# Optimization experiments

Measured on AMD Instinct MI355X. Metric: run time of the kernel, lower is better.

The kernel has to match this reference:

```python
import jax, jax.numpy as jnp
import numpy as np

# 5x5 binomial Gaussian kernel, normalized by 256
_K = jnp.array([[1., 4., 6., 4., 1.],
                [4., 16., 24., 16., 4.],
                [6., 24., 36., 24., 6.],
                [4., 16., 24., 16., 4.],
                [1., 4., 6., 4., 1.]], dtype=jnp.float32) / 256.0


def _gauss_conv(img, kernel):
    # depthwise 5x5 conv with reflect padding 2 (same spatial size)
    C = img.shape[1]
    p = jnp.pad(img, ((0, 0), (0, 0), (2, 2), (2, 2)), mode='reflect')
    return jax.lax.conv_general_dilated(
        p, kernel, window_strides=(1, 1), padding='VALID',
        dimension_numbers=('NCHW', 'OIHW', 'NCHW'),
        feature_group_count=C)


def _lap_pyramid(img, kernel, max_levels=5):
    pyr = []
    cur = img
    for _ in range(max_levels):  # fixed small loop over pyramid levels
        H, W = cur.shape[2], cur.shape[3]
        cur = cur[:, :, :H - H % 2, :W - W % 2]  # crop to even size
        down = _gauss_conv(cur, kernel)[:, :, ::2, ::2]
        up = jnp.zeros(cur.shape, cur.dtype).at[:, :, ::2, ::2].set(down * 4.0)
        up = _gauss_conv(up, kernel)
        pyr.append(cur - up)
        cur = down
    return pyr


def setup_inputs() -> dict:
    key = jax.random.key(0)
    k1, k2 = jax.random.split(key)
    predict = jax.random.uniform(k1, (16, 3, 512, 512), dtype=jnp.float32)
    target = jax.random.uniform(k2, (16, 3, 512, 512), dtype=jnp.float32)
    return {"predict": predict, "target": target}


def reference(predict, target):
    C = predict.shape[1]
    kernel = jnp.tile(_K.astype(predict.dtype)[None, None], (C, 1, 1, 1))  # [C,1,5,5]
    pyr_p = _lap_pyramid(predict, kernel, 5)
    pyr_t = _lap_pyramid(target, kernel, 5)
    weights = (1.0, 2.0, 4.0, 8.0, 16.0)
    loss = jnp.asarray(0.0, predict.dtype)
    for w, a, b in zip(weights, pyr_p, pyr_t):
        loss = loss + w * jnp.mean(jnp.abs(a - b))  # F.l1_loss (mean reduction)
    return loss
```

## Files before the change

### kernel.cpp

```cpp
#include <hip/hip_runtime.h>


__device__ __forceinline__ int reflect_i(int m, int S) {
    if (m < 0) m = -m;
    if (m >= S) m = 2 * S - 2 - m;
    return m;
}

__device__ __forceinline__ void wg_barrier() {
    asm volatile("s_waitcnt lgkmcnt(0)" ::: "memory");
    __builtin_amdgcn_s_barrier();
}

#define LGKM0 asm volatile("s_waitcnt lgkmcnt(0)" ::: "memory")

template <int N>
__device__ __forceinline__ void wait_vm() {
    if constexpr (N == 0)      asm volatile("s_waitcnt vmcnt(0)" ::: "memory");
    else if constexpr (N == 1) asm volatile("s_waitcnt vmcnt(1)" ::: "memory");
    else if constexpr (N == 2) asm volatile("s_waitcnt vmcnt(2)" ::: "memory");
    else if constexpr (N == 4) asm volatile("s_waitcnt vmcnt(4)" ::: "memory");
    else if constexpr (N == 8) asm volatile("s_waitcnt vmcnt(8)" ::: "memory");
}

__device__ __forceinline__ void gld16(const void* g, void* l) {
    __builtin_amdgcn_global_load_lds(
        (const __attribute__((address_space(1))) void*)g,
        (__attribute__((address_space(3))) void*)l, 16, 0, 0);
}

__device__ __forceinline__ int swz4(int B) { return B ^ (((B >> 7) & 7) << 4); }

template <int S, int ISL0, int DH>
__global__ __launch_bounds__(256, 2)
void pyr_kernel(const float* __restrict__ a, const float* __restrict__ b,
                float* __restrict__ dwn, float* __restrict__ acc, float scale) {
    constexpr int D = S / 2;
    constexpr int CPL = S / 128;
    constexpr int W = 2 * CPL + 3;
    constexpr int ROWB = (CPL == 4) ? 2048 : 1024;
    constexpr int SLOT = ROWB * (ISL0 ? 2 : 1);
    constexpr int OPS = (CPL == 4) ? (ISL0 ? 4 : 2) : 1;
    constexpr int NRS = D / DH;

    __shared__ float4 ringmem[4 * 4 * SLOT / 16];
    const int wv = threadIdx.x >> 6;
    const int lane = threadIdx.x & 63;
    char* ring = (char*)ringmem + wv * (4 * SLOT);

    const int wid = blockIdx.x * 4 + wv;
    const int rs = wid % NRS;
    const int n = wid / NRS;
    const int R0 = rs * DH;
    const size_t gbase = (size_t)n * S * S;

    auto stage_row = [&](int s) {
        int gr = reflect_i(2 * R0 - 4 + s, S);
        const char* ga = (const char*)(a + gbase + (size_t)gr * S);
        char* la = ring + (s & 3) * SLOT;
        if constexpr (CPL == 4) {
            gld16(ga + swz4(16 * lane), la);
            gld16(ga + swz4(16 * lane + 1024), la + 1024);
        } else if constexpr (CPL == 2) {
            gld16(ga + 16 * lane, la);
        } else {
            gld16(ga + 16 * (lane & 31), la);
        }
        if constexpr (ISL0) {
            const char* gb = (const char*)(b + gbase + (size_t)gr * S);
            gld16(gb + swz4(16 * lane), la + ROWB);
            gld16(gb + swz4(16 * lane + 1024), la + ROWB + 1024);
        }
    };

    auto read_win = [&](int s, float* w) {
        const char* pa = ring + (s & 3) * SLOT;
        if constexpr (CPL == 4) {
            int bl = 32 * lane;
            float2 lo = *(const float2*)(pa + swz4(lane ? bl - 8 : 0));
            float4 m0 = *(const float4*)(pa + swz4(bl));
            float4 m1 = *(const float4*)(pa + swz4(bl + 16));
            float hi = *(const float*)(pa + swz4(lane == 63 ? 2032 : bl + 32));
            w[0]=lo.x; w[1]=lo.y; w[2]=m0.x; w[3]=m0.y; w[4]=m0.z; w[5]=m0.w;
            w[6]=m1.x; w[7]=m1.y; w[8]=m1.z; w[9]=m1.w; w[10]=hi;
            if constexpr (ISL0) {
                const char* pb = pa + ROWB;
                float2 l2 = *(const float2*)(pb + swz4(lane ? bl - 8 : 0));
                float4 t0 = *(const float4*)(pb + swz4(bl));
                float4 t1 = *(const float4*)(pb + swz4(bl + 16));
                float h2 = *(const float*)(pb + swz4(lane == 63 ? 2032 : bl + 32));
                w[0]-=l2.x; w[1]-=l2.y; w[2]-=t0.x; w[3]-=t0.y; w[4]-=t0.z;
                w[5]-=t0.w; w[6]-=t1.x; w[7]-=t1.y; w[8]-=t1.z; w[9]-=t1.w; w[10]-=h2;
            }
        } else if constexpr (CPL == 2) {
            int bl = 16 * lane;
            float2 lo = *(const float2*)(pa + (lane ? bl - 8 : 0));
            float4 m0 = *(const float4*)(pa + bl);
            float hi = *(const float*)(pa + (lane == 63 ? 1008 : bl + 16));
            w[0]=lo.x; w[1]=lo.y; w[2]=m0.x; w[3]=m0.y; w[4]=m0.z; w[5]=m0.w; w[6]=hi;
        } else {
            int bl = 8 * lane;
            float2 lo = *(const float2*)(pa + (lane ? bl - 8 : 0));
            float2 m0 = *(const float2*)(pa + bl);
            float hi = *(const float*)(pa + (lane == 63 ? 496 : bl + 8));
            w[0]=lo.x; w[1]=lo.y; w[2]=m0.x; w[3]=m0.y; w[4]=hi;
        }
        if (lane == 0)  { w[0] = w[4]; w[1] = w[3]; }
        if (lane == 63) { w[W - 1] = w[W - 3]; }
    };

    auto hof = [&](const float* w, float* h) {
        #pragma unroll
        for (int j = 0; j < CPL; j++)
            h[j] = w[2*j] + 4.f*w[2*j+1] + 6.f*w[2*j+2] + 4.f*w[2*j+3] + w[2*j+4];
    };

    float hA[CPL], hB[CPL], hC[CPL], hD[CPL], hE[CPL];
    float cEv1[2*CPL], cEv2[2*CPL], cOd1[2*CPL];
    float ex0[CPL] = {}, ex1[CPL] = {}, ox0[CPL] = {}, ox1[CPL] = {};
    float sum = 0.f;
    float* dbase = dwn + (size_t)n * D * D;

    stage_row(0); stage_row(1); stage_row(2); stage_row(3);
    wait_vm<OPS>();
    {
        float w[W];
        read_win(0, w); hof(w, hA);
        read_win(1, w); hof(w, hB);
        read_win(2, w); hof(w, hC);
    }
    LGKM0;
    stage_row(4); stage_row(5); stage_row(6);

    #pragma unroll
    for (int j = 0; j <= DH + 1; ++j) {
        const int m = R0 - 1 + j;
        if (j <= DH) wait_vm<2 * OPS>(); else wait_vm<0>();

        float w3[W], w4[W];
        read_win(2 * j + 3, w3); hof(w3, hD);
        read_win(2 * j + 4, w4); hof(w4, hE);

        float d[CPL], dl[CPL], dr[CPL], ex2[CPL], ox2[CPL];
        #pragma unroll
        for (int q = 0; q < CPL; q++)
            d[q] = (hA[q] + 4.f*hB[q] + 6.f*hC[q] + 4.f*hD[q] + hE[q]) * (1.f / 256.f);
        float dli = __shfl_up(d[CPL - 1], 1, 64);
        float dri = __shfl_down(d[0], 1, 64);
        dl[0] = (lane == 0) ? ((CPL > 1) ? d[1] : dri) : dli;
        #pragma unroll
        for (int q = 1; q < CPL; q++) dl[q] = d[q - 1];
        dr[CPL - 1] = (lane == 63) ? d[CPL - 1] : dri;
        #pragma unroll
        for (int q = 0; q < CPL - 1; q++) dr[q] = d[q + 1];
        #pragma unroll
        for (int q = 0; q < CPL; q++) {
            ex2[q] = 0.125f * (dl[q] + 6.f * d[q] + dr[q]);
            ox2[q] = 0.5f * (d[q] + dr[q]);
        }

        if (j >= 1 && j <= DH) {
            char* dst = (char*)(dbase + (size_t)m * D + CPL * lane);
            if constexpr (CPL == 4)      *(float4*)dst = make_float4(d[0], d[1], d[2], d[3]);
            else if constexpr (CPL == 2) *(float2*)dst = make_float2(d[0], d[1]);
            else                         *(float*)dst = d[0];
        }

        if (j >= 2) {
            const int me = m - 1;
            #pragma unroll
            for (int q = 0; q < CPL; q++) {
                float eA = (me == 0) ? ex2[q] : ex0[q];
                float oA = (me == 0) ? ox2[q] : ox0[q];
                float eC = (me == D - 1) ? ex1[q] : ex2[q];
                float oC = (me == D - 1) ? ox1[q] : ox2[q];
                float uee = 0.125f * (eA + 6.f * ex1[q] + eC);
                float ueo = 0.125f * (oA + 6.f * ox1[q] + oC);
                float uoe = 0.5f * (ex1[q] + eC);
                float uoo = 0.5f * (ox1[q] + oC);
                sum += fabsf(cEv2[2*q]   - uee) + fabsf(cEv2[2*q+1] - ueo)
                     + fabsf(cOd1[2*q]   - uoe) + fabsf(cOd1[2*q+1] - uoo);
            }
        }

        #pragma unroll
        for (int q = 0; q < CPL; q++) {
            ex0[q] = ex1[q]; ex1[q] = ex2[q];
            ox0[q] = ox1[q]; ox1[q] = ox2[q];
            hA[q] = hC[q]; hB[q] = hD[q]; hC[q] = hE[q];
        }
        #pragma unroll
        for (int q = 0; q < 2 * CPL; q++) {
            cEv2[q] = cEv1[q];
            cEv1[q] = w4[2 + q];
            cOd1[q] = w3[2 + q];
        }

        if (j <= DH - 1) {
            LGKM0;
            stage_row(2 * j + 7);
            stage_row(2 * j + 8);
        }
    }

    #pragma unroll
    for (int o = 32; o > 0; o >>= 1) sum += __shfl_down(sum, o, 64);
    if (lane == 0) atomicAdd(&acc[wid & 63], sum * scale);
}

__device__ float level_in_lds(const float* cur, float* h, float* dn,
                              int S, int tid, int nt) {
    const int D = S >> 1;
    for (int i = tid; i < S * D; i += nt) {
        int r = i / D, xh = i % D;
        int c0 = reflect_i(2 * xh - 2, S), c1 = reflect_i(2 * xh - 1, S);
        int c3 = 2 * xh + 1, c4 = reflect_i(2 * xh + 2, S);
        const float* row = cur + r * S;
        h[i] = row[c0] + 4.f * row[c1] + 6.f * row[2 * xh] + 4.f * row[c3] + row[c4];
    }
    wg_barrier();
    for (int i = tid; i < D * D; i += nt) {
        int yh = i / D, xh = i % D;
        int r0 = reflect_i(2 * yh - 2, S), r1 = reflect_i(2 * yh - 1, S);
        int r3 = 2 * yh + 1, r4 = reflect_i(2 * yh + 2, S);
        dn[i] = (h[r0 * D + xh] + 4.f * h[r1 * D + xh] + 6.f * h[2 * yh * D + xh]
               + 4.f * h[r3 * D + xh] + h[r4 * D + xh]) * (1.f / 256.f);
    }
    wg_barrier();
    float sum = 0.f;
    for (int i = tid; i < D * D; i += nt) {
        int yh2 = i / D, q = i % D;
        int rm = (yh2 == 0) ? 1 : yh2 - 1;
        int rp = (yh2 == D - 1) ? D - 1 : yh2 + 1;
        int cm = (q == 0) ? 1 : q - 1;
        int cp = (q == D - 1) ? D - 1 : q + 1;
        float A00 = dn[rm * D + cm], A01 = dn[rm * D + q], A02 = dn[rm * D + cp];
        float A10 = dn[yh2 * D + cm], A11 = dn[yh2 * D + q], A12 = dn[yh2 * D + cp];
        float A20 = dn[rp * D + cm], A21 = dn[rp * D + q], A22 = dn[rp * D + cp];
        float ex0 = (A00 + 6.f * A01 + A02) * 0.125f;
        float ex1 = (A10 + 6.f * A11 + A12) * 0.125f;
        float ex2 = (A20 + 6.f * A21 + A22) * 0.125f;
        float ox0 = (A01 + A02) * 0.5f;
        float ox1 = (A11 + A12) * 0.5f;
        float ox2 = (A21 + A22) * 0.5f;
        float uee = (ex0 + 6.f * ex1 + ex2) * 0.125f;
        float ueo = (ox0 + 6.f * ox1 + ox2) * 0.125f;
        float uoe = (ex1 + ex2) * 0.5f;
        float uoo = (ox1 + ox2) * 0.5f;
        const float* c0 = cur + (2 * yh2) * S + 2 * q;
        sum += fabsf(c0[0] - uee) + fabsf(c0[1] - ueo)
             + fabsf(c0[S] - uoe) + fabsf(c0[S + 1] - uoo);
    }
    wg_barrier();
    return sum;
}

__global__ __launch_bounds__(256)
void tail_kernel(const float* __restrict__ d2, float* __restrict__ acc,
                 float s3, float s4) {
    __shared__ float cur[64 * 64];
    __shared__ float hbuf[64 * 32];
    __shared__ float dn3[32 * 32];
    __shared__ float dn4[16 * 16];
    int n = blockIdx.x, tid = threadIdx.x;
    const float4* src = (const float4*)(d2 + (size_t)n * 64 * 64);
    for (int i = tid; i < 64 * 16; i += 256) ((float4*)cur)[i] = src[i];
    wg_barrier();
    float sum = level_in_lds(cur, hbuf, dn3, 64, tid, 256) * s3;
    sum += level_in_lds(dn3, hbuf, dn4, 32, tid, 256) * s4;
    #pragma unroll
    for (int o = 32; o > 0; o >>= 1) sum += __shfl_down(sum, o, 64);
    __shared__ float s[4];
    int lane = tid & 63, w = tid >> 6;
    if (lane == 0) s[w] = sum;
    wg_barrier();
    if (tid == 0) atomicAdd(&acc[n & 63], s[0] + s[1] + s[2] + s[3]);
}

__global__ void finish_kernel(const float* __restrict__ acc, float* __restrict__ out) {
    float v = acc[threadIdx.x];
    #pragma unroll
    for (int o = 32; o > 0; o >>= 1) v += __shfl_down(v, o, 64);
    if (threadIdx.x == 0) out[0] = v;
}

extern "C" void kernel_launch(void* const* d_in, const int* in_sizes, int n_in,
                              void* d_out, int out_size, void* d_ws, size_t ws_size,
                              hipStream_t stream) {
    const float* p = (const float*)d_in[0];
    const float* t = (const float*)d_in[1];
    float* out = (float*)d_out;
    float* acc = (float*)d_ws;
    float* dn0 = acc + 64;
    float* dn1 = dn0 + (size_t)48 * 256 * 256;
    float* dn2 = dn1 + (size_t)48 * 128 * 128;

    hipMemsetAsync(acc, 0, 64 * sizeof(float), stream);

    const int N = 48;

    pyr_kernel<512, 1, 8><<<384, 256, 0, stream>>>(
        p, t, dn0, acc, 1.f / (float)(N * 512 * 512));
    pyr_kernel<256, 0, 4><<<384, 256, 0, stream>>>(
        dn0, nullptr, dn1, acc, 2.f / (float)(N * 256 * 256));
    pyr_kernel<128, 0, 4><<<192, 256, 0, stream>>>(
        dn1, nullptr, dn2, acc, 4.f / (float)(N * 128 * 128));
    tail_kernel<<<N, 256, 0, stream>>>(dn2, acc,
                                       8.f / (float)(N * 64 * 64),
                                       16.f / (float)(N * 32 * 32));
    finish_kernel<<<1, 64, 0, stream>>>(acc, out);
}
```

Baseline: 67.85 us.

## Replace overlapping LDS window reads with aligned loads and lane shuffles

Each lane now reads only its own aligned float4 chunks from LDS and gets horizontal neighbours by cross-lane shuffles, instead of overlapping unaligned window reads that needed an XOR swizzle. For the 512-wide level the columns are interleaved, so a lane owns two separate halves of the row. The stored downsampled output is split into two float2 stores to match that layout. Levels 256 and 128 also process more rows per wave with half as many blocks, which cuts halo re-reads but lowers parallelism. The cost is extra shuffle instructions and more complex boundary handling.

```diff
diff --git a/kernel.cpp b/kernel.cpp
--- a/kernel.cpp
+++ b/kernel.cpp
@@ -29,15 +29,12 @@
         (__attribute__((address_space(3))) void*)l, 16, 0, 0);
 }
 
-__device__ __forceinline__ int swz4(int B) { return B ^ (((B >> 7) & 7) << 4); }
-
 template <int S, int ISL0, int DH>
 __global__ __launch_bounds__(256, 2)
 void pyr_kernel(const float* __restrict__ a, const float* __restrict__ b,
                 float* __restrict__ dwn, float* __restrict__ acc, float scale) {
     constexpr int D = S / 2;
     constexpr int CPL = S / 128;
-    constexpr int W = 2 * CPL + 3;
     constexpr int ROWB = (CPL == 4) ? 2048 : 1024;
     constexpr int SLOT = ROWB * (ISL0 ? 2 : 1);
     constexpr int OPS = (CPL == 4) ? (ISL0 ? 4 : 2) : 1;
@@ -59,8 +56,8 @@
         const char* ga = (const char*)(a + gbase + (size_t)gr * S);
         char* la = ring + (s & 3) * SLOT;
         if constexpr (CPL == 4) {
-            gld16(ga + swz4(16 * lane), la);
-            gld16(ga + swz4(16 * lane + 1024), la + 1024);
+            gld16(ga + 16 * lane, la);
+            gld16(ga + 16 * lane + 1024, la + 1024);
         } else if constexpr (CPL == 2) {
             gld16(ga + 16 * lane, la);
         } else {
@@ -68,67 +65,79 @@
         }
         if constexpr (ISL0) {
             const char* gb = (const char*)(b + gbase + (size_t)gr * S);
-            gld16(gb + swz4(16 * lane), la + ROWB);
-            gld16(gb + swz4(16 * lane + 1024), la + ROWB + 1024);
+            gld16(gb + 16 * lane, la + ROWB);
+            gld16(gb + 16 * lane + 1024, la + ROWB + 1024);
         }
     };
 
-    auto read_win = [&](int s, float* w) {
+    auto proc_row = [&](int s, float* c, float* h) {
         const char* pa = ring + (s & 3) * SLOT;
         if constexpr (CPL == 4) {
-            int bl = 32 * lane;
-            float2 lo = *(const float2*)(pa + swz4(lane ? bl - 8 : 0));
-            float4 m0 = *(const float4*)(pa + swz4(bl));
-            float4 m1 = *(const float4*)(pa + swz4(bl + 16));
-            float hi = *(const float*)(pa + swz4(lane == 63 ? 2032 : bl + 32));
-            w[0]=lo.x; w[1]=lo.y; w[2]=m0.x; w[3]=m0.y; w[4]=m0.z; w[5]=m0.w;
-            w[6]=m1.x; w[7]=m1.y; w[8]=m1.z; w[9]=m1.w; w[10]=hi;
+            float4 x0 = *(const float4*)(pa + 16 * lane);
+            float4 x1 = *(const float4*)(pa + 1024 + 16 * lane);
             if constexpr (ISL0) {
                 const char* pb = pa + ROWB;
-                float2 l2 = *(const float2*)(pb + swz4(lane ? bl - 8 : 0));
-                float4 t0 = *(const float4*)(pb + swz4(bl));
-                float4 t1 = *(const float4*)(pb + swz4(bl + 16));
-                float h2 = *(const float*)(pb + swz4(lane == 63 ? 2032 : bl + 32));
-                w[0]-=l2.x; w[1]-=l2.y; w[2]-=t0.x; w[3]-=t0.y; w[4]-=t0.z;
-                w[5]-=t0.w; w[6]-=t1.x; w[7]-=t1.y; w[8]-=t1.z; w[9]-=t1.w; w[10]-=h2;
+                float4 y0 = *(const float4*)(pb + 16 * lane);
+                float4 y1 = *(const float4*)(pb + 1024 + 16 * lane);
+                x0.x -= y0.x; x0.y -= y0.y; x0.z -= y0.z; x0.w -= y0.w;
+                x1.x -= y1.x; x1.y -= y1.y; x1.z -= y1.z; x1.w -= y1.w;
             }
+            c[0]=x0.x; c[1]=x0.y; c[2]=x0.z; c[3]=x0.w;
+            c[4]=x1.x; c[5]=x1.y; c[6]=x1.z; c[7]=x1.w;
+            float lu2  = __shfl_up(x0.z, 1, 64);
+            float lu3  = __shfl_up(x0.w, 1, 64);
+            float rd0  = __shfl_down(x0.x, 1, 64);
+            float bcA  = __shfl(x1.x, 0, 64);
+            float lu2b = __shfl_up(x1.z, 1, 64);
+            float lu3b = __shfl_up(x1.w, 1, 64);
+            float rd0b = __shfl_down(x1.x, 1, 64);
+            float bcZ  = __shfl(x0.z, 63, 64);
+            float bcW  = __shfl(x0.w, 63, 64);
+            float w0 = (lane == 0) ? x0.z : lu2;
+            float w1 = (lane == 0) ? x0.y : lu3;
+            float w6 = (lane == 63) ? bcA : rd0;
+            float v0 = (lane == 0) ? bcZ : lu2b;
+            float v1 = (lane == 0) ? bcW : lu3b;
+            float v6 = (lane == 63) ? x1.z : rd0b;
+            h[0] = w0 + 4.f*w1 + 6.f*x0.x + 4.f*x0.y + x0.z;
+            h[1] = x0.x + 4.f*x0.y + 6.f*x0.z + 4.f*x0.w + w6;
+            h[2] = v0 + 4.f*v1 + 6.f*x1.x + 4.f*x1.y + x1.z;
+            h[3] = x1.x + 4.f*x1.y + 6.f*x1.z + 4.f*x1.w + v6;
         } else if constexpr (CPL == 2) {
-            int bl = 16 * lane;
-            float2 lo = *(const float2*)(pa + (lane ? bl - 8 : 0));
-            float4 m0 = *(const float4*)(pa + bl);
-            float hi = *(const float*)(pa + (lane == 63 ? 1008 : bl + 16));
-            w[0]=lo.x; w[1]=lo.y; w[2]=m0.x; w[3]=m0.y; w[4]=m0.z; w[5]=m0.w; w[6]=hi;
+            float4 x0 = *(const float4*)(pa + 16 * lane);
+            c[0]=x0.x; c[1]=x0.y; c[2]=x0.z; c[3]=x0.w;
+            float lu2 = __shfl_up(x0.z, 1, 64);
+            float lu3 = __shfl_up(x0.w, 1, 64);
+            float rd0 = __shfl_down(x0.x, 1, 64);
+            float w0 = (lane == 0) ? x0.z : lu2;
+            float w1 = (lane == 0) ? x0.y : lu3;
+            float w6 = (lane == 63) ? x0.z : rd0;
+            h[0] = w0 + 4.f*w1 + 6.f*x0.x + 4.f*x0.y + x0.z;
+            h[1] = x0.x + 4.f*x0.y + 6.f*x0.z + 4.f*x0.w + w6;
         } else {
-            int bl = 8 * lane;
-            float2 lo = *(const float2*)(pa + (lane ? bl - 8 : 0));
-            float2 m0 = *(const float2*)(pa + bl);
-            float hi = *(const float*)(pa + (lane == 63 ? 496 : bl + 8));
-            w[0]=lo.x; w[1]=lo.y; w[2]=m0.x; w[3]=m0.y; w[4]=hi;
-        }
-        if (lane == 0)  { w[0] = w[4]; w[1] = w[3]; }
-        if (lane == 63) { w[W - 1] = w[W - 3]; }
+            float2 x0 = *(const float2*)(pa + 8 * lane);
+            c[0]=x0.x; c[1]=x0.y;
+            float lu0 = __shfl_up(x0.x, 1, 64);
+            float lu1 = __shfl_up(x0.y, 1, 64);
+            float rd0 = __shfl_down(x0.x, 1, 64);
+            float w0 = (lane == 0) ? rd0 : lu0;
+            float w1 = (lane == 0) ? x0.y : lu1;
+            float w4 = (lane == 63) ? x0.x : rd0;
+            h[0] = w0 + 4.f*w1 + 6.f*x0.x + 4.f*x0.y + w4;
+        }
     };
 
-    auto hof = [&](const float* w, float* h) {
-        #pragma unroll
-        for (int j = 0; j < CPL; j++)
-            h[j] = w[2*j] + 4.f*w[2*j+1] + 6.f*w[2*j+2] + 4.f*w[2*j+3] + w[2*j+4];
-    };
-
     float hA[CPL], hB[CPL], hC[CPL], hD[CPL], hE[CPL];
-    float cEv1[2*CPL], cEv2[2*CPL], cOd1[2*CPL];
+    float cEv1[2*CPL], cEv2[2*CPL], cOd1[2*CPL], dump[2*CPL];
     float ex0[CPL] = {}, ex1[CPL] = {}, ox0[CPL] = {}, ox1[CPL] = {};
     float sum = 0.f;
     float* dbase = dwn + (size_t)n * D * D;
 
     stage_row(0); stage_row(1); stage_row(2); stage_row(3);
     wait_vm<OPS>();
-    {
-        float w[W];
-        read_win(0, w); hof(w, hA);
-        read_win(1, w); hof(w, hB);
-        read_win(2, w); hof(w, hC);
-    }
+    proc_row(0, dump, hA);
+    proc_row(1, dump, hB);
+    proc_row(2, dump, hC);
     LGKM0;
     stage_row(4); stage_row(5); stage_row(6);
 
@@ -137,22 +146,43 @@
         const int m = R0 - 1 + j;
         if (j <= DH) wait_vm<2 * OPS>(); else wait_vm<0>();
 
-        float w3[W], w4[W];
-        read_win(2 * j + 3, w3); hof(w3, hD);
-        read_win(2 * j + 4, w4); hof(w4, hE);
+        float c3[2*CPL], c4[2*CPL];
+        proc_row(2 * j + 3, c3, hD);
+        proc_row(2 * j + 4, c4, hE);
 
         float d[CPL], dl[CPL], dr[CPL], ex2[CPL], ox2[CPL];
         #pragma unroll
         for (int q = 0; q < CPL; q++)
             d[q] = (hA[q] + 4.f*hB[q] + 6.f*hC[q] + 4.f*hD[q] + hE[q]) * (1.f / 256.f);
-        float dli = __shfl_up(d[CPL - 1], 1, 64);
-        float dri = __shfl_down(d[0], 1, 64);
-        dl[0] = (lane == 0) ? ((CPL > 1) ? d[1] : dri) : dli;
-        #pragma unroll
-        for (int q = 1; q < CPL; q++) dl[q] = d[q - 1];
-        dr[CPL - 1] = (lane == 63) ? d[CPL - 1] : dri;
-        #pragma unroll
-        for (int q = 0; q < CPL - 1; q++) dr[q] = d[q + 1];
+
+        if constexpr (CPL == 4) {
+            float su1 = __shfl_up(d[1], 1, 64);
+            float su3 = __shfl_up(d[3], 1, 64);
+            float sd0 = __shfl_down(d[0], 1, 64);
+            float sd2 = __shfl_down(d[2], 1, 64);
+            float bc1 = __shfl(d[1], 63, 64);
+            float bc2 = __shfl(d[2], 0, 64);
+            dl[0] = (lane == 0) ? d[1] : su1;
+            dl[1] = d[0];
+            dl[2] = (lane == 0) ? bc1 : su3;
+            dl[3] = d[2];
+            dr[0] = d[1];
+            dr[1] = (lane == 63) ? bc2 : sd0;
+            dr[2] = d[3];
+            dr[3] = (lane == 63) ? d[3] : sd2;
+        } else if constexpr (CPL == 2) {
+            float su1 = __shfl_up(d[1], 1, 64);
+            float sd0 = __shfl_down(d[0], 1, 64);
+            dl[0] = (lane == 0) ? d[1] : su1;
+            dl[1] = d[0];
+            dr[0] = d[1];
+            dr[1] = (lane == 63) ? d[1] : sd0;
+        } else {
+            float su = __shfl_up(d[0], 1, 64);
+            float sd = __shfl_down(d[0], 1, 64);
+            dl[0] = (lane == 0) ? sd : su;
+            dr[0] = (lane == 63) ? d[0] : sd;
+        }
         #pragma unroll
         for (int q = 0; q < CPL; q++) {
             ex2[q] = 0.125f * (dl[q] + 6.f * d[q] + dr[q]);
@@ -160,10 +190,14 @@
         }
 
         if (j >= 1 && j <= DH) {
-            char* dst = (char*)(dbase + (size_t)m * D + CPL * lane);
-            if constexpr (CPL == 4)      *(float4*)dst = make_float4(d[0], d[1], d[2], d[3]);
-            else if constexpr (CPL == 2) *(float2*)dst = make_float2(d[0], d[1]);
-            else                         *(float*)dst = d[0];
+            if constexpr (CPL == 4) {
+                *(float2*)(dbase + (size_t)m * D + 2 * lane) = make_float2(d[0], d[1]);
+                *(float2*)(dbase + (size_t)m * D + D / 2 + 2 * lane) = make_float2(d[2], d[3]);
+            } else if constexpr (CPL == 2) {
+                *(float2*)(dbase + (size_t)m * D + 2 * lane) = make_float2(d[0], d[1]);
+            } else {
+                dbase[(size_t)m * D + lane] = d[0];
+            }
         }
 
         if (j >= 2) {
@@ -192,8 +226,8 @@
         #pragma unroll
         for (int q = 0; q < 2 * CPL; q++) {
             cEv2[q] = cEv1[q];
-            cEv1[q] = w4[2 + q];
-            cOd1[q] = w3[2 + q];
+            cEv1[q] = c4[q];
+            cOd1[q] = c3[q];
         }
 
         if (j <= DH - 1) {
@@ -301,9 +335,9 @@
 
     pyr_kernel<512, 1, 8><<<384, 256, 0, stream>>>(
         p, t, dn0, acc, 1.f / (float)(N * 512 * 512));
-    pyr_kernel<256, 0, 4><<<384, 256, 0, stream>>>(
+    pyr_kernel<256, 0, 8><<<192, 256, 0, stream>>>(
         dn0, nullptr, dn1, acc, 2.f / (float)(N * 256 * 256));
-    pyr_kernel<128, 0, 4><<<192, 256, 0, stream>>>(
+    pyr_kernel<128, 0, 8><<<96, 256, 0, stream>>>(
         dn1, nullptr, dn2, acc, 4.f / (float)(N * 128 * 128));
     tail_kernel<<<N, 256, 0, stream>>>(dn2, acc,
                                        8.f / (float)(N * 64 * 64),
```

After: 66.26 us. -2.3%, faster.
